# Performance work log

Hardware: AMD Instinct MI355X
Metric: run time of the kernel (lower is better)

Reference implementation:

```python
import jax, jax.numpy as jnp
import numpy as np

N_HEAD = 16
N_FEAT = 1024
D_K = N_FEAT // N_HEAD


def rtt_half(x):
    x1, x2 = x[..., : x.shape[-1] // 2], x[..., x.shape[-1] // 2 :]
    return jnp.concatenate([-x2, x1], axis=-1)


def setup_inputs() -> dict:
    key = jax.random.key(0)
    ks = jax.random.split(key, 16)
    B, T, D = 4, 2048, N_FEAT
    inp = {
        "query": jax.random.normal(ks[0], (B, T, D), jnp.float32),
        "key": jax.random.normal(ks[1], (B, T, D), jnp.float32),
        "value": jax.random.normal(ks[2], (B, T, D), jnp.float32),
        "cos": jax.random.uniform(ks[3], (T, 1, D_K), jnp.float32),
        "sin": jax.random.uniform(ks[4], (T, 1, D_K), jnp.float32),
        "mask": jnp.zeros((B, T, T), jnp.bool_),
    }
    s = 1.0 / np.sqrt(D)
    inp["Wq"] = jax.random.uniform(ks[5], (D, D), jnp.float32, -s, s)
    inp["bq"] = jax.random.uniform(ks[6], (D,), jnp.float32, -s, s)
    inp["Wk"] = jax.random.uniform(ks[7], (D, D), jnp.float32, -s, s)
    inp["bk"] = jax.random.uniform(ks[8], (D,), jnp.float32, -s, s)
    inp["Wv"] = jax.random.uniform(ks[9], (D, D), jnp.float32, -s, s)
    inp["bv"] = jax.random.uniform(ks[10], (D,), jnp.float32, -s, s)
    inp["Wo"] = jax.random.uniform(ks[11], (D, D), jnp.float32, -s, s)
    inp["bo"] = jax.random.uniform(ks[12], (D,), jnp.float32, -s, s)
    return inp


def reference(query, key, value, cos, sin, mask, Wq, bq, Wk, bk, Wv, bv, Wo, bo):
    B, T, D = query.shape
    h, d_k = N_HEAD, D_K
    # QKV projections (torch Linear: x @ W.T + b), reshape to (B,T,h,d_k)
    q = (query @ Wq.T + bq).reshape(B, T, h, d_k)
    k = (key @ Wk.T + bk).reshape(B, T, h, d_k)
    v = (value @ Wv.T + bv).reshape(B, T, h, d_k)
    # RoPE: cos/sin sliced to T, broadcast (T,1,d_k) over (B,T,h,d_k)
    c, s = cos[:T], sin[:T]
    q = q * c + rtt_half(q) * s
    k = k * c + rtt_half(k) * s
    # attention scores (B,h,T,T)
    scores = jnp.einsum("bqhd,bkhd->bhqk", q, k) / np.sqrt(d_k).astype(jnp.float32)
    scores = jnp.where(mask[:, None, :, :], -jnp.inf, scores)
    attn = jax.nn.softmax(scores, axis=-1)
    out = jnp.einsum("bhqk,bkhd->bqhd", attn, v).reshape(B, T, D)
    return out @ Wo.T + bo
```

## Files before the change

kernel.cpp:

```cpp
#include <hip/hip_runtime.h>

#define B_SZ 4
#define T_SZ 2048
#define D_SZ 1024
#define H_SZ 16
#define DK_SZ 64
#define M_SZ (B_SZ * T_SZ)

typedef __attribute__((ext_vector_type(8))) short bf16x8;
typedef __attribute__((ext_vector_type(4))) short bf16x4;
typedef __attribute__((ext_vector_type(4))) float f32x4;

union fui { float f; unsigned u; };

static __device__ inline short f2bf(float x) {
    union { float f; unsigned u; } v; v.f = x;
    unsigned r = v.u + 0x7fff + ((v.u >> 16) & 1);
    return (short)(r >> 16);
}
static __device__ inline void split1(float f, short* h, short* l) {
    fui a; a.f = f;
    *h = (short)(a.u >> 16);
    fui t; t.u = a.u & 0xffff0000u;
    fui r; r.f = f - t.f;
    *l = (short)(r.u >> 16);
}

#define MFMA16(a, b, c) __builtin_amdgcn_mfma_f32_16x16x32_bf16((a), (b), (c), 0, 0, 0)

#define GLDS16(g, l) __builtin_amdgcn_global_load_lds(                        \
    (const __attribute__((address_space(1))) unsigned int*)(g),               \
    (__attribute__((address_space(3))) unsigned int*)(l), 16, 0, 0)

static __device__ inline void split8(float4 f0, float4 f1, bf16x8* hi, bf16x8* lo)
{
    fui a[8];
    a[0].f = f0.x; a[1].f = f0.y; a[2].f = f0.z; a[3].f = f0.w;
    a[4].f = f1.x; a[5].f = f1.y; a[6].f = f1.z; a[7].f = f1.w;
    union { unsigned w[4]; bf16x8 v; } H, L;
#pragma unroll
    for (int p = 0; p < 4; ++p)
        H.w[p] = __builtin_amdgcn_perm(a[2 * p + 1].u, a[2 * p].u, 0x07060302);
#pragma unroll
    for (int j = 0; j < 8; ++j) {
        fui t; t.u = a[j].u & 0xffff0000u;
        fui r; r.f = a[j].f - t.f;
        a[j].u = r.u;
    }
#pragma unroll
    for (int p = 0; p < 4; ++p)
        L.w[p] = __builtin_amdgcn_perm(a[2 * p + 1].u, a[2 * p].u, 0x07060302);
    *hi = H.v; *lo = L.v;
}

__global__ __launch_bounds__(256)
void wsplit_kernel(const float* __restrict__ W, short* __restrict__ Wh,
                   short* __restrict__ Wl)
{
    const int i = blockIdx.x * 256 + threadIdx.x;
    float4 f = ((const float4*)W)[i];
    fui a[4]; a[0].f = f.x; a[1].f = f.y; a[2].f = f.z; a[3].f = f.w;
    union { short s[4]; short4 v; } H, L;
#pragma unroll
    for (int j = 0; j < 4; ++j) {
        H.s[j] = (short)(a[j].u >> 16);
        fui t; t.u = a[j].u & 0xffff0000u;
        fui r; r.f = a[j].f - t.f;
        L.s[j] = (short)(r.u >> 16);
    }
    ((short4*)Wh)[i] = H.v;
    ((short4*)Wl)[i] = L.v;
}

__global__ __launch_bounds__(256)
void mask_flags_kernel(const unsigned char* __restrict__ mask, int* __restrict__ flags)
{
    const int f = blockIdx.x * 4 + (threadIdx.x >> 6);
    const int lane = threadIdx.x & 63;
    const int b = f >> 10, qt = (f >> 5) & 31, kt = f & 31;
    const unsigned char* base = mask + ((size_t)b * T_SZ + qt * 64) * T_SZ + kt * 64;
    bool nz = false;
#pragma unroll
    for (int i = 0; i < 4; ++i) {
        const int c = lane + 64 * i;
        const int row = c >> 2, off = (c & 3) * 16;
        uint4 v = *(const uint4*)(base + (size_t)row * T_SZ + off);
        nz |= ((v.x | v.y | v.z | v.w) != 0);
    }
    unsigned long long bal = __ballot(nz);
    if (lane == 0) flags[f] = (bal != 0) ? 1 : 0;
}

__global__ __launch_bounds__(256)
void qkv_mfma_kernel(const float* __restrict__ Aq, const float* __restrict__ Ak,
                     const float* __restrict__ Av,
                     const short* __restrict__ Wqh, const short* __restrict__ Wql,
                     const short* __restrict__ Wkh, const short* __restrict__ Wkl,
                     const short* __restrict__ Wvh, const short* __restrict__ Wvl,
                     const float* __restrict__ bq, const float* __restrict__ bk,
                     const float* __restrict__ bv,
                     const float* __restrict__ cosb, const float* __restrict__ sinb,
                     short* __restrict__ Qh, short* __restrict__ Ql,
                     short* __restrict__ Kh, short* __restrict__ Kl,
                     short* __restrict__ Vb)
{
    __shared__ __align__(16) short Whs[128 * 32];
    __shared__ __align__(16) short Wls[128 * 32];

    const int which = blockIdx.y >> 3;
    const int m0 = blockIdx.x * 128, n0 = (blockIdx.y & 7) * 128;
    const float* A  = (which == 0) ? Aq  : (which == 1) ? Ak  : Av;
    const short* Wh = (which == 0) ? Wqh : (which == 1) ? Wkh : Wvh;
    const short* Wl = (which == 0) ? Wql : (which == 1) ? Wkl : Wvl;
    const float* bias = (which == 0) ? bq : (which == 1) ? bk : bv;

    const int tid = threadIdx.x;
    const int wv = tid >> 6, lane = tid & 63;
    const int wm = wv >> 1, wn = wv & 1;
    const int l15 = lane & 15, quad = lane >> 4;

    f32x4 acc[4][4];
#pragma unroll
    for (int mt = 0; mt < 4; ++mt)
#pragma unroll
        for (int nt = 0; nt < 4; ++nt)
            acc[mt][nt] = (f32x4){0.f, 0.f, 0.f, 0.f};

    const short* whg = Wh + (size_t)(n0 + wv * 32 + (lane >> 2)) * D_SZ + (lane & 3) * 8;
    const short* wlg = Wl + (size_t)(n0 + wv * 32 + (lane >> 2)) * D_SZ + (lane & 3) * 8;
    short* whl0 = &Whs[wv * 1024];
    short* wll0 = &Wls[wv * 1024];

    const float* aB[4];
#pragma unroll
    for (int mt = 0; mt < 4; ++mt)
        aB[mt] = A + (size_t)(m0 + wm * 64 + mt * 16 + l15) * D_SZ + quad * 8;

    for (int k0 = 0; k0 < D_SZ; k0 += 32) {
        float4 af0[4], af1[4];
#pragma unroll
        for (int mt = 0; mt < 4; ++mt) {
            af0[mt] = *(const float4*)(aB[mt] + k0);
            af1[mt] = *(const float4*)(aB[mt] + k0 + 4);
        }
        __syncthreads();
        GLDS16(whg + k0,             whl0);
        GLDS16(whg + 16 * D_SZ + k0, whl0 + 512);
        GLDS16(wlg + k0,             wll0);
        GLDS16(wlg + 16 * D_SZ + k0, wll0 + 512);

        bf16x8 ah[4], al[4];
#pragma unroll
        for (int mt = 0; mt < 4; ++mt)
            split8(af0[mt], af1[mt], &ah[mt], &al[mt]);

        __syncthreads();

#pragma unroll
        for (int nt = 0; nt < 4; ++nt) {
            const int brow = (wn * 64 + nt * 16 + l15) * 32 + quad * 8;
            const bf16x8 bh = *(const bf16x8*)&Whs[brow];
            const bf16x8 bl = *(const bf16x8*)&Wls[brow];
#pragma unroll
            for (int mt = 0; mt < 4; ++mt) {
                acc[mt][nt] = MFMA16(ah[mt], bh, acc[mt][nt]);
                acc[mt][nt] = MFMA16(al[mt], bh, acc[mt][nt]);
                acc[mt][nt] = MFMA16(ah[mt], bl, acc[mt][nt]);
            }
        }
    }

    const int hh = ((blockIdx.y & 7) << 1) + wn;
    if (which < 2) {
        short* Hd = (which == 0) ? Qh : Kh;
        short* Ld = (which == 0) ? Ql : Kl;
        const float qscale = (which == 0) ? 0.125f : 1.0f;
#pragma unroll
        for (int mt = 0; mt < 4; ++mt)
#pragma unroll
            for (int p = 0; p < 2; ++p) {
                const int d1 = p * 16 + l15, d2 = d1 + 32;
                const int col1 = n0 + wn * 64 + d1;
                const float b1 = bias[col1], b2 = bias[col1 + 32];
#pragma unroll
                for (int r = 0; r < 4; ++r) {
                    const int m = m0 + wm * 64 + mt * 16 + quad * 4 + r;
                    const int bb = m >> 11, tg = m & (T_SZ - 1);
                    const float c1 = cosb[tg * 64 + d1], s1 = sinb[tg * 64 + d1];
                    const float c2 = cosb[tg * 64 + d2], s2 = sinb[tg * 64 + d2];
                    const float x1 = acc[mt][p][r] + b1;
                    const float x2 = acc[mt][p + 2][r] + b2;
                    const float y1 = (x1 * c1 - x2 * s1) * qscale;
                    const float y2 = (x2 * c2 + x1 * s2) * qscale;
                    const size_t base = (((size_t)(bb * H_SZ + hh)) * T_SZ + tg) * 64;
                    short h_, l_;
                    split1(y1, &h_, &l_); Hd[base + d1] = h_; Ld[base + d1] = l_;
                    split1(y2, &h_, &l_); Hd[base + d2] = h_; Ld[base + d2] = l_;
                }
            }
    } else {
#pragma unroll
        for (int nt = 0; nt < 4; ++nt) {
            const int d = nt * 16 + l15;
            const float bvv = bias[n0 + wn * 64 + d];
#pragma unroll
            for (int mt = 0; mt < 4; ++mt)
#pragma unroll
                for (int r = 0; r < 4; ++r) {
                    const int m = m0 + wm * 64 + mt * 16 + quad * 4 + r;
                    const int bb = m >> 11, tg = m & (T_SZ - 1);
                    Vb[(((size_t)(bb * H_SZ + hh)) * T_SZ + tg) * 64 + d] =
                        f2bf(acc[mt][nt][r] + bvv);
                }
        }
    }
}

__global__ __launch_bounds__(256)
void gemm_out_kernel(const float* __restrict__ A, const short* __restrict__ Wh,
                     const short* __restrict__ Wl, const float* __restrict__ bias,
                     float* __restrict__ C)
{
    __shared__ __align__(16) short Whs[128 * 32];
    __shared__ __align__(16) short Wls[128 * 32];

    const int m0 = blockIdx.x * 128, n0 = blockIdx.y * 128;
    const int tid = threadIdx.x;
    const int wv = tid >> 6, lane = tid & 63;
    const int wm = wv >> 1, wn = wv & 1;
    const int l15 = lane & 15, quad = lane >> 4;

    f32x4 acc[4][4];
#pragma unroll
    for (int mt = 0; mt < 4; ++mt)
#pragma unroll
        for (int nt = 0; nt < 4; ++nt)
            acc[mt][nt] = (f32x4){0.f, 0.f, 0.f, 0.f};

    const short* whg = Wh + (size_t)(n0 + wv * 32 + (lane >> 2)) * D_SZ + (lane & 3) * 8;
    const short* wlg = Wl + (size_t)(n0 + wv * 32 + (lane >> 2)) * D_SZ + (lane & 3) * 8;
    short* whl0 = &Whs[wv * 1024];
    short* wll0 = &Wls[wv * 1024];

    const float* aB[4];
#pragma unroll
    for (int mt = 0; mt < 4; ++mt)
        aB[mt] = A + (size_t)(m0 + wm * 64 + mt * 16 + l15) * D_SZ + quad * 8;

    for (int k0 = 0; k0 < D_SZ; k0 += 32) {
        float4 af0[4], af1[4];
#pragma unroll
        for (int mt = 0; mt < 4; ++mt) {
            af0[mt] = *(const float4*)(aB[mt] + k0);
            af1[mt] = *(const float4*)(aB[mt] + k0 + 4);
        }
        __syncthreads();
        GLDS16(whg + k0,             whl0);
        GLDS16(whg + 16 * D_SZ + k0, whl0 + 512);
        GLDS16(wlg + k0,             wll0);
        GLDS16(wlg + 16 * D_SZ + k0, wll0 + 512);

        bf16x8 ah[4], al[4];
#pragma unroll
        for (int mt = 0; mt < 4; ++mt)
            split8(af0[mt], af1[mt], &ah[mt], &al[mt]);

        __syncthreads();

#pragma unroll
        for (int nt = 0; nt < 4; ++nt) {
            const int brow = (wn * 64 + nt * 16 + l15) * 32 + quad * 8;
            const bf16x8 bh = *(const bf16x8*)&Whs[brow];
            const bf16x8 bl = *(const bf16x8*)&Wls[brow];
#pragma unroll
            for (int mt = 0; mt < 4; ++mt) {
                acc[mt][nt] = MFMA16(ah[mt], bh, acc[mt][nt]);
                acc[mt][nt] = MFMA16(al[mt], bh, acc[mt][nt]);
                acc[mt][nt] = MFMA16(ah[mt], bl, acc[mt][nt]);
            }
        }
    }

#pragma unroll
    for (int nt = 0; nt < 4; ++nt) {
        const int col = n0 + wn * 64 + nt * 16 + l15;
        const float bvv = bias[col];
#pragma unroll
        for (int mt = 0; mt < 4; ++mt)
#pragma unroll
            for (int r = 0; r < 4; ++r) {
                const int m = m0 + wm * 64 + mt * 16 + quad * 4 + r;
                C[(size_t)m * D_SZ + col] = acc[mt][nt][r] + bvv;
            }
    }
}

__global__ __launch_bounds__(256)
void attn_mfma_kernel(const short* __restrict__ Qhg, const short* __restrict__ Qlg,
                      const short* __restrict__ Khg, const short* __restrict__ Klg,
                      const short* __restrict__ Vg,
                      const unsigned char* __restrict__ mask,
                      const int* __restrict__ flags,
                      float* __restrict__ ob)
{
    __shared__ __align__(16) short Khs[64 * 72];
    __shared__ __align__(16) short Kls[64 * 72];
    __shared__ __align__(16) short Vt[64 * 72];
    __shared__ __align__(16) short Ps[4 * 16 * 72];

    const int bh = blockIdx.y;
    const int b = bh >> 4, h = bh & 15;
    const int q0 = blockIdx.x * 64;
    const int tid = threadIdx.x;
    const int wv = tid >> 6, lane = tid & 63;
    const int l15 = lane & 15, quad = lane >> 4;

    const short* qhp = Qhg + ((size_t)bh * T_SZ + q0 + wv * 16 + l15) * 64 + quad * 8;
    const short* qlp = Qlg + ((size_t)bh * T_SZ + q0 + wv * 16 + l15) * 64 + quad * 8;
    bf16x8 qh[2], ql[2];
#pragma unroll
    for (int s = 0; s < 2; ++s) {
        qh[s] = *(const bf16x8*)(qhp + 32 * s);
        ql[s] = *(const bf16x8*)(qlp + 32 * s);
    }

    f32x4 accO[4];
#pragma unroll
    for (int nt = 0; nt < 4; ++nt) accO[nt] = (f32x4){0.f, 0.f, 0.f, 0.f};
    float m_i[4], l_i[4];
#pragma unroll
    for (int r = 0; r < 4; ++r) { m_i[r] = -1e30f; l_i[r] = 0.f; }

    const short* khb = Khg + (size_t)bh * T_SZ * 64;
    const short* klb = Klg + (size_t)bh * T_SZ * 64;
    const short* vb  = Vg  + (size_t)bh * T_SZ * 64;
    const unsigned char* mbase = mask + ((size_t)b * T_SZ + q0) * T_SZ;
    const int* frow = flags + ((size_t)b * 32 + blockIdx.x) * 32;

    const int vt0 = (tid >> 4) * 4, vd0 = (tid & 15) * 4;
    short* pw = &Ps[wv * 16 * 72];

    for (int kti = 0; kti < 32; ++kti) {
        const int kt = kti * 64;
        __syncthreads();
#pragma unroll
        for (int jj = 0; jj < 4; ++jj) {
            const short* g = (jj < 2) ? khb : klb;
            short* lds = (jj < 2) ? Khs : Kls;
            const int cc = tid + 256 * (jj & 1);
            const int row = cc >> 3, off = (cc & 7) * 8;
            *(bf16x8*)(lds + row * 72 + off) =
                *(const bf16x8*)(g + (size_t)(kt + row) * 64 + off);
        }
        {
            uint2 rv[4];
#pragma unroll
            for (int i = 0; i < 4; ++i)
                rv[i] = *(const uint2*)(vb + (size_t)(kt + vt0 + i) * 64 + vd0);
#pragma unroll
            for (int c = 0; c < 4; ++c) {
                const int k = c >> 1;
                const unsigned sel = (c & 1) ? 0x07060302u : 0x05040100u;
                const unsigned lo0 = k ? rv[0].y : rv[0].x;
                const unsigned lo1 = k ? rv[1].y : rv[1].x;
                const unsigned lo2 = k ? rv[2].y : rv[2].x;
                const unsigned lo3 = k ? rv[3].y : rv[3].x;
                uint2 o;
                o.x = __builtin_amdgcn_perm(lo1, lo0, sel);
                o.y = __builtin_amdgcn_perm(lo3, lo2, sel);
                *(uint2*)&Vt[(vd0 + c) * 72 + vt0] = o;
            }
        }
        __syncthreads();

        f32x4 accS[4];
#pragma unroll
        for (int nt = 0; nt < 4; ++nt) {
            f32x4 acc = (f32x4){0.f, 0.f, 0.f, 0.f};
#pragma unroll
            for (int s = 0; s < 2; ++s) {
                const bf16x8 kh = *(const bf16x8*)&Khs[(nt * 16 + l15) * 72 + 32 * s + quad * 8];
                const bf16x8 kl = *(const bf16x8*)&Kls[(nt * 16 + l15) * 72 + 32 * s + quad * 8];
                acc = MFMA16(qh[s], kh, acc);
                acc = MFMA16(ql[s], kh, acc);
                acc = MFMA16(qh[s], kl, acc);
            }
            accS[nt] = acc;
        }

        float sv[4][4];
        if (frow[kti]) {
#pragma unroll
            for (int nt = 0; nt < 4; ++nt)
#pragma unroll
                for (int r = 0; r < 4; ++r) {
                    const unsigned char mb =
                        mbase[(size_t)(wv * 16 + quad * 4 + r) * T_SZ + kt + nt * 16 + l15];
                    sv[nt][r] = mb ? -1e30f : accS[nt][r];
                }
        } else {
#pragma unroll
            for (int nt = 0; nt < 4; ++nt)
#pragma unroll
                for (int r = 0; r < 4; ++r)
                    sv[nt][r] = accS[nt][r];
        }

        float rmax[4];
#pragma unroll
        for (int r = 0; r < 4; ++r)
            rmax[r] = fmaxf(fmaxf(sv[0][r], sv[1][r]), fmaxf(sv[2][r], sv[3][r]));
#pragma unroll
        for (int off = 1; off < 16; off <<= 1)
#pragma unroll
            for (int r = 0; r < 4; ++r)
                rmax[r] = fmaxf(rmax[r], __shfl_xor(rmax[r], off, 64));

        float alpha[4];
#pragma unroll
        for (int r = 0; r < 4; ++r) {
            const float mnew = fmaxf(m_i[r], rmax[r]);
            alpha[r] = __expf(m_i[r] - mnew);
            m_i[r] = mnew;
        }
        float lsum[4] = {0.f, 0.f, 0.f, 0.f};
#pragma unroll
        for (int nt = 0; nt < 4; ++nt)
#pragma unroll
            for (int r = 0; r < 4; ++r) {
                const float p = __expf(sv[nt][r] - m_i[r]);
                sv[nt][r] = p;
                lsum[r] += p;
            }
#pragma unroll
        for (int r = 0; r < 4; ++r)
            l_i[r] = l_i[r] * alpha[r] + lsum[r];

#pragma unroll
        for (int nt = 0; nt < 4; ++nt)
#pragma unroll
            for (int r = 0; r < 4; ++r) {
                fui u; u.f = sv[nt][r];
                pw[(quad * 4 + r) * 72 + nt * 16 + l15] = (short)((u.u + 0x8000u) >> 16);
            }

#pragma unroll
        for (int nt = 0; nt < 4; ++nt)
#pragma unroll
            for (int r = 0; r < 4; ++r)
                accO[nt][r] *= alpha[r];

        bf16x8 pa[2];
#pragma unroll
        for (int s = 0; s < 2; ++s)
            pa[s] = *(const bf16x8*)&pw[l15 * 72 + 32 * s + quad * 8];
#pragma unroll
        for (int nt = 0; nt < 4; ++nt)
#pragma unroll
            for (int s = 0; s < 2; ++s) {
                const bf16x8 vf = *(const bf16x8*)&Vt[(nt * 16 + l15) * 72 + 32 * s + quad * 8];
                accO[nt] = MFMA16(pa[s], vf, accO[nt]);
            }
    }

#pragma unroll
    for (int off = 1; off < 16; off <<= 1)
#pragma unroll
        for (int r = 0; r < 4; ++r)
            l_i[r] += __shfl_xor(l_i[r], off, 64);

#pragma unroll
    for (int r = 0; r < 4; ++r) {
        const float inv = 1.f / l_i[r];
        const int t = q0 + wv * 16 + quad * 4 + r;
        float* orow = ob + ((size_t)(b * T_SZ + t)) * D_SZ + h * DK_SZ;
#pragma unroll
        for (int nt = 0; nt < 4; ++nt)
            orow[nt * 16 + l15] = accO[nt][r] * inv;
    }
}

extern "C" void kernel_launch(void* const* d_in, const int* in_sizes, int n_in,
                              void* d_out, int out_size, void* d_ws, size_t ws_size,
                              hipStream_t stream)
{
    const float* query = (const float*)d_in[0];
    const float* key   = (const float*)d_in[1];
    const float* value = (const float*)d_in[2];
    const float* cosb  = (const float*)d_in[3];
    const float* sinb  = (const float*)d_in[4];
    const unsigned char* mask = (const unsigned char*)d_in[5];
    const float* Wq = (const float*)d_in[6];
    const float* bq = (const float*)d_in[7];
    const float* Wk = (const float*)d_in[8];
    const float* bk = (const float*)d_in[9];
    const float* Wv = (const float*)d_in[10];
    const float* bv = (const float*)d_in[11];
    const float* Wo = (const float*)d_in[12];
    const float* bo = (const float*)d_in[13];
    float* out = (float*)d_out;

    short* sp = (short*)d_ws;
    const size_t eb = (size_t)B_SZ * H_SZ * T_SZ * DK_SZ;
    short* Qh = sp;          short* Ql = sp + eb;
    short* Kh = sp + 2 * eb; short* Kl = sp + 3 * eb;
    short* Vb = sp + 4 * eb;
    float* abuf = (float*)(sp + 5 * eb);
    short* wsp = (short*)(abuf + eb);
    const size_t wlen = (size_t)D_SZ * D_SZ;
    short* wqh = wsp;            short* wql = wsp + wlen;
    short* wkh = wsp + 2 * wlen; short* wkl = wsp + 3 * wlen;
    short* wvh = wsp + 4 * wlen; short* wvl = wsp + 5 * wlen;
    short* woh = wsp + 6 * wlen; short* wol = wsp + 7 * wlen;
    int* flags = (int*)(wsp + 8 * wlen);

    const int wsBlocks = (int)(wlen / 4 / 256);
    wsplit_kernel<<<wsBlocks, 256, 0, stream>>>(Wq, wqh, wql);
    wsplit_kernel<<<wsBlocks, 256, 0, stream>>>(Wk, wkh, wkl);
    wsplit_kernel<<<wsBlocks, 256, 0, stream>>>(Wv, wvh, wvl);
    wsplit_kernel<<<wsBlocks, 256, 0, stream>>>(Wo, woh, wol);

    mask_flags_kernel<<<1024, 256, 0, stream>>>(mask, flags);

    qkv_mfma_kernel<<<dim3(M_SZ / 128, 24), 256, 0, stream>>>(
        query, key, value, wqh, wql, wkh, wkl, wvh, wvl,
        bq, bk, bv, cosb, sinb, Qh, Ql, Kh, Kl, Vb);

    attn_mfma_kernel<<<dim3(T_SZ / 64, B_SZ * H_SZ), 256, 0, stream>>>(
        Qh, Ql, Kh, Kl, Vb, mask, flags, abuf);

    gemm_out_kernel<<<dim3(M_SZ / 128, D_SZ / 128), 256, 0, stream>>>(
        abuf, woh, wol, bo, out);
}
```

Baseline: 781.3 us.

## Process 128 queries per attention block with two sub-tiles per wave

```diff
diff --git a/kernel.cpp b/kernel.cpp
--- a/kernel.cpp
+++ b/kernel.cpp
@@ -310,34 +310,40 @@
 
     const int bh = blockIdx.y;
     const int b = bh >> 4, h = bh & 15;
-    const int q0 = blockIdx.x * 64;
+    const int q0 = blockIdx.x * 128;
     const int tid = threadIdx.x;
     const int wv = tid >> 6, lane = tid & 63;
     const int l15 = lane & 15, quad = lane >> 4;
 
-    const short* qhp = Qhg + ((size_t)bh * T_SZ + q0 + wv * 16 + l15) * 64 + quad * 8;
-    const short* qlp = Qlg + ((size_t)bh * T_SZ + q0 + wv * 16 + l15) * 64 + quad * 8;
-    bf16x8 qh[2], ql[2];
-#pragma unroll
-    for (int s = 0; s < 2; ++s) {
-        qh[s] = *(const bf16x8*)(qhp + 32 * s);
-        ql[s] = *(const bf16x8*)(qlp + 32 * s);
-    }
-
-    f32x4 accO[4];
-#pragma unroll
-    for (int nt = 0; nt < 4; ++nt) accO[nt] = (f32x4){0.f, 0.f, 0.f, 0.f};
-    float m_i[4], l_i[4];
-#pragma unroll
-    for (int r = 0; r < 4; ++r) { m_i[r] = -1e30f; l_i[r] = 0.f; }
+    bf16x8 qh[2][2], ql[2][2];
+#pragma unroll
+    for (int sub = 0; sub < 2; ++sub) {
+        const short* qhp = Qhg + ((size_t)bh * T_SZ + q0 + wv * 32 + sub * 16 + l15) * 64 + quad * 8;
+        const short* qlp = Qlg + ((size_t)bh * T_SZ + q0 + wv * 32 + sub * 16 + l15) * 64 + quad * 8;
+#pragma unroll
+        for (int s = 0; s < 2; ++s) {
+            qh[sub][s] = *(const bf16x8*)(qhp + 32 * s);
+            ql[sub][s] = *(const bf16x8*)(qlp + 32 * s);
+        }
+    }
+
+    f32x4 accO[2][4];
+    float m_i[2][4], l_i[2][4];
+#pragma unroll
+    for (int sub = 0; sub < 2; ++sub)
+#pragma unroll
+        for (int nt = 0; nt < 4; ++nt) {
+            accO[sub][nt] = (f32x4){0.f, 0.f, 0.f, 0.f};
+            m_i[sub][nt] = -1e30f; l_i[sub][nt] = 0.f;
+        }
 
     const short* khb = Khg + (size_t)bh * T_SZ * 64;
     const short* klb = Klg + (size_t)bh * T_SZ * 64;
     const short* vb  = Vg  + (size_t)bh * T_SZ * 64;
     const unsigned char* mbase = mask + ((size_t)b * T_SZ + q0) * T_SZ;
-    const int* frow = flags + ((size_t)b * 32 + blockIdx.x) * 32;
-
-    const int vt0 = (tid >> 4) * 4, vd0 = (tid & 15) * 4;
+    const int* frow = flags + ((size_t)b * 32 + blockIdx.x * 2 + (wv >> 1)) * 32;
+
+    const int vt0 = (tid & 15) * 4, vd0 = (tid >> 4) * 4;
     short* pw = &Ps[wv * 16 * 72];
 
     for (int kti = 0; kti < 32; ++kti) {
@@ -373,110 +379,129 @@
         }
         __syncthreads();
 
-        f32x4 accS[4];
-#pragma unroll
-        for (int nt = 0; nt < 4; ++nt) {
-            f32x4 acc = (f32x4){0.f, 0.f, 0.f, 0.f};
+        f32x4 accS[2][4];
+#pragma unroll
+        for (int sub = 0; sub < 2; ++sub)
+#pragma unroll
+            for (int nt = 0; nt < 4; ++nt)
+                accS[sub][nt] = (f32x4){0.f, 0.f, 0.f, 0.f};
+
+        __builtin_amdgcn_s_setprio(1);
+#pragma unroll
+        for (int nt = 0; nt < 4; ++nt)
 #pragma unroll
             for (int s = 0; s < 2; ++s) {
                 const bf16x8 kh = *(const bf16x8*)&Khs[(nt * 16 + l15) * 72 + 32 * s + quad * 8];
                 const bf16x8 kl = *(const bf16x8*)&Kls[(nt * 16 + l15) * 72 + 32 * s + quad * 8];
-                acc = MFMA16(qh[s], kh, acc);
-                acc = MFMA16(ql[s], kh, acc);
-                acc = MFMA16(qh[s], kl, acc);
-            }
-            accS[nt] = acc;
-        }
-
-        float sv[4][4];
-        if (frow[kti]) {
+#pragma unroll
+                for (int sub = 0; sub < 2; ++sub) {
+                    accS[sub][nt] = MFMA16(qh[sub][s], kh, accS[sub][nt]);
+                    accS[sub][nt] = MFMA16(ql[sub][s], kh, accS[sub][nt]);
+                    accS[sub][nt] = MFMA16(qh[sub][s], kl, accS[sub][nt]);
+                }
+            }
+        __builtin_amdgcn_s_setprio(0);
+
+        const int msk = frow[kti];
+        bf16x8 pa[2][2];
+
+#pragma unroll
+        for (int sub = 0; sub < 2; ++sub) {
+            float sv[4][4];
+            if (msk) {
+#pragma unroll
+                for (int nt = 0; nt < 4; ++nt)
+#pragma unroll
+                    for (int r = 0; r < 4; ++r) {
+                        const unsigned char mb =
+                            mbase[(size_t)(wv * 32 + sub * 16 + quad * 4 + r) * T_SZ + kt + nt * 16 + l15];
+                        sv[nt][r] = mb ? -1e30f : accS[sub][nt][r];
+                    }
+            } else {
+#pragma unroll
+                for (int nt = 0; nt < 4; ++nt)
+#pragma unroll
+                    for (int r = 0; r < 4; ++r)
+                        sv[nt][r] = accS[sub][nt][r];
+            }
+
+            float rmax[4];
+#pragma unroll
+            for (int r = 0; r < 4; ++r)
+                rmax[r] = fmaxf(fmaxf(sv[0][r], sv[1][r]), fmaxf(sv[2][r], sv[3][r]));
+#pragma unroll
+            for (int off = 1; off < 16; off <<= 1)
+#pragma unroll
+                for (int r = 0; r < 4; ++r)
+                    rmax[r] = fmaxf(rmax[r], __shfl_xor(rmax[r], off, 64));
+
+            float alpha[4];
+#pragma unroll
+            for (int r = 0; r < 4; ++r) {
+                const float mnew = fmaxf(m_i[sub][r], rmax[r]);
+                alpha[r] = __expf(m_i[sub][r] - mnew);
+                m_i[sub][r] = mnew;
+            }
+            float lsum[4] = {0.f, 0.f, 0.f, 0.f};
 #pragma unroll
             for (int nt = 0; nt < 4; ++nt)
 #pragma unroll
                 for (int r = 0; r < 4; ++r) {
-                    const unsigned char mb =
-                        mbase[(size_t)(wv * 16 + quad * 4 + r) * T_SZ + kt + nt * 16 + l15];
-                    sv[nt][r] = mb ? -1e30f : accS[nt][r];
+                    const float p = __expf(sv[nt][r] - m_i[sub][r]);
+                    sv[nt][r] = p;
+                    lsum[r] += p;
                 }
-        } else {
+#pragma unroll
+            for (int r = 0; r < 4; ++r)
+                l_i[sub][r] = l_i[sub][r] * alpha[r] + lsum[r];
+
 #pragma unroll
             for (int nt = 0; nt < 4; ++nt)
 #pragma unroll
+                for (int r = 0; r < 4; ++r) {
+                    fui u; u.f = sv[nt][r];
+                    pw[(quad * 4 + r) * 72 + nt * 16 + l15] = (short)((u.u + 0x8000u) >> 16);
+                }
+#pragma unroll
+            for (int s = 0; s < 2; ++s)
+                pa[sub][s] = *(const bf16x8*)&pw[l15 * 72 + 32 * s + quad * 8];
+
+#pragma unroll
+            for (int nt = 0; nt < 4; ++nt)
+#pragma unroll
                 for (int r = 0; r < 4; ++r)
-                    sv[nt][r] = accS[nt][r];
-        }
-
-        float rmax[4];
-#pragma unroll
-        for (int r = 0; r < 4; ++r)
-            rmax[r] = fmaxf(fmaxf(sv[0][r], sv[1][r]), fmaxf(sv[2][r], sv[3][r]));
-#pragma unroll
-        for (int off = 1; off < 16; off <<= 1)
-#pragma unroll
-            for (int r = 0; r < 4; ++r)
-                rmax[r] = fmaxf(rmax[r], __shfl_xor(rmax[r], off, 64));
-
-        float alpha[4];
-#pragma unroll
-        for (int r = 0; r < 4; ++r) {
-            const float mnew = fmaxf(m_i[r], rmax[r]);
-            alpha[r] = __expf(m_i[r] - mnew);
-            m_i[r] = mnew;
-        }
-        float lsum[4] = {0.f, 0.f, 0.f, 0.f};
-#pragma unroll
-        for (int nt = 0; nt < 4; ++nt)
-#pragma unroll
-            for (int r = 0; r < 4; ++r) {
-                const float p = __expf(sv[nt][r] - m_i[r]);
-                sv[nt][r] = p;
-                lsum[r] += p;
-            }
-#pragma unroll
-        for (int r = 0; r < 4; ++r)
-            l_i[r] = l_i[r] * alpha[r] + lsum[r];
-
-#pragma unroll
-        for (int nt = 0; nt < 4; ++nt)
-#pragma unroll
-            for (int r = 0; r < 4; ++r) {
-                fui u; u.f = sv[nt][r];
-                pw[(quad * 4 + r) * 72 + nt * 16 + l15] = (short)((u.u + 0x8000u) >> 16);
-            }
-
-#pragma unroll
-        for (int nt = 0; nt < 4; ++nt)
-#pragma unroll
-            for (int r = 0; r < 4; ++r)
-                accO[nt][r] *= alpha[r];
-
-        bf16x8 pa[2];
-#pragma unroll
-        for (int s = 0; s < 2; ++s)
-            pa[s] = *(const bf16x8*)&pw[l15 * 72 + 32 * s + quad * 8];
+                    accO[sub][nt][r] *= alpha[r];
+        }
+
+        __builtin_amdgcn_s_setprio(1);
 #pragma unroll
         for (int nt = 0; nt < 4; ++nt)
 #pragma unroll
             for (int s = 0; s < 2; ++s) {
                 const bf16x8 vf = *(const bf16x8*)&Vt[(nt * 16 + l15) * 72 + 32 * s + quad * 8];
-                accO[nt] = MFMA16(pa[s], vf, accO[nt]);
-            }
-    }
-
-#pragma unroll
-    for (int off = 1; off < 16; off <<= 1)
-#pragma unroll
-        for (int r = 0; r < 4; ++r)
-            l_i[r] += __shfl_xor(l_i[r], off, 64);
-
-#pragma unroll
-    for (int r = 0; r < 4; ++r) {
-        const float inv = 1.f / l_i[r];
-        const int t = q0 + wv * 16 + quad * 4 + r;
-        float* orow = ob + ((size_t)(b * T_SZ + t)) * D_SZ + h * DK_SZ;
-#pragma unroll
-        for (int nt = 0; nt < 4; ++nt)
-            orow[nt * 16 + l15] = accO[nt][r] * inv;
+                accO[0][nt] = MFMA16(pa[0][s], vf, accO[0][nt]);
+                accO[1][nt] = MFMA16(pa[1][s], vf, accO[1][nt]);
+            }
+        __builtin_amdgcn_s_setprio(0);
+    }
+
+#pragma unroll
+    for (int sub = 0; sub < 2; ++sub) {
+#pragma unroll
+        for (int off = 1; off < 16; off <<= 1)
+#pragma unroll
+            for (int r = 0; r < 4; ++r)
+                l_i[sub][r] += __shfl_xor(l_i[sub][r], off, 64);
+
+#pragma unroll
+        for (int r = 0; r < 4; ++r) {
+            const float inv = 1.f / l_i[sub][r];
+            const int t = q0 + wv * 32 + sub * 16 + quad * 4 + r;
+            float* orow = ob + ((size_t)(b * T_SZ + t)) * D_SZ + h * DK_SZ;
+#pragma unroll
+            for (int nt = 0; nt < 4; ++nt)
+                orow[nt * 16 + l15] = accO[sub][nt][r] * inv;
+        }
     }
 }
 
@@ -526,7 +551,7 @@
         query, key, value, wqh, wql, wkh, wkl, wvh, wvl,
         bq, bk, bv, cosb, sinb, Qh, Ql, Kh, Kl, Vb);
 
-    attn_mfma_kernel<<<dim3(T_SZ / 64, B_SZ * H_SZ), 256, 0, stream>>>(
+    attn_mfma_kernel<<<dim3(T_SZ / 128, B_SZ * H_SZ), 256, 0, stream>>>(
         Qh, Ql, Kh, Kl, Vb, mask, flags, abuf);
 
     gemm_out_kernel<<<dim3(M_SZ / 128, D_SZ / 128), 256, 0, stream>>>(
```

Result: slower. 891.1 us (+14.1%).
